# Kernel tuning notes

Hardware: AMD Instinct MI355X
Metric: run time of the kernel (lower is better)

## Reference

```python
import jax, jax.numpy as jnp
import numpy as np

K = 3          # kernel_size
DIL = 2        # dilation
PAD = 2        # unfold padding
EPS = 1e-5     # InstanceNorm eps


def setup_inputs() -> dict:
    key = jax.random.key(0)
    ks = jax.random.split(key, 6)
    b, c, h, w = 8, 128, 128, 128
    c_red = c // 8                      # reduction_ratio = 8
    k2 = K * K
    x = jax.random.normal(ks[0], (b, c, h, w), dtype=jnp.float32)
    # conv1: 1x1, channels -> channels//8, no bias
    w1 = jax.random.normal(ks[1], (c_red, c), dtype=jnp.float32) * (1.0 / np.sqrt(c))
    # InstanceNorm2d affine params
    in_gamma = jnp.ones((c_red,), dtype=jnp.float32)
    in_beta = jnp.zeros((c_red,), dtype=jnp.float32)
    # conv2: 1x1, channels//8 -> k^2 * groups (groups == channels since group_channels=1)
    w2 = jax.random.normal(ks[2], (k2 * c, c_red), dtype=jnp.float32) * (1.0 / np.sqrt(c_red))
    b2 = jnp.zeros((k2 * c,), dtype=jnp.float32)
    return {"x": x, "w1": w1, "in_gamma": in_gamma, "in_beta": in_beta, "w2": w2, "b2": b2}


def reference(x, w1, in_gamma, in_beta, w2, b2):
    b, c, h, w = x.shape
    k2 = K * K
    # --- weight generation branch (stride == 1, ZeroPad2d arg is 0 -> no-op) ---
    t = jnp.einsum('oc,bchw->bohw', w1, x)                      # 1x1 conv, no bias
    mean = t.mean(axis=(2, 3), keepdims=True)                   # InstanceNorm2d (biased var)
    var = t.var(axis=(2, 3), keepdims=True)
    t = (t - mean) * jax.lax.rsqrt(var + EPS)
    t = t * in_gamma[None, :, None, None] + in_beta[None, :, None, None]
    t = jax.nn.relu(t)
    wgt = jnp.einsum('oc,bchw->bohw', w2, t) + b2[None, :, None, None]
    wgt = wgt.reshape(b, c, k2, h, w)                           # (b, groups=c, k^2, h, w)
    # --- unfold: dilated 3x3 patches, padding=2 -> same spatial size ---
    xp = jnp.pad(x, ((0, 0), (0, 0), (PAD, PAD), (PAD, PAD)))
    patches = jnp.stack(
        [xp[:, :, DIL * i:DIL * i + h, DIL * j:DIL * j + w]
         for i in range(K) for j in range(K)], axis=2)          # (b, c, k^2, h, w)
    # --- dynamic-weight multiply + reduce over kernel taps ---
    return (wgt * patches).sum(axis=2)                          # (b, c, h, w)
```

## Files before the change

kernel.cpp:

```cpp
#include <hip/hip_runtime.h>

#define BB   8
#define CC   128
#define CR   16
#define HH   128
#define WW   128
#define HWSZ 16384
#define K2   9
#define NFRAG 72

typedef _Float16 f16x8 __attribute__((ext_vector_type(8)));
typedef float    f32x4 __attribute__((ext_vector_type(4)));

#define WS_PART   0
#define WS_TRAWLO 16384
#define WS_TRAWHI 540672
#define WS_TNLO   1064960
#define WS_TNHI   1589248
#define WS_AFRAG  2113536

__global__ __launch_bounds__(256) void k_conv1(const float* __restrict__ x,
                                               const float* __restrict__ w1,
                                               const float* __restrict__ w2,
                                               const float* __restrict__ b2,
                                               float* __restrict__ ws) {
    const int bid = blockIdx.x;
    const int tid = threadIdx.x;

    if (bid >= 512) {
        const int id = (bid - 512) * 256 + tid;
        if (id >= NFRAG * 64) return;
        const int lane = id & 63;
        const int frag = id >> 6;
        const int ct = frag / 9, k = frag - ct * 9;
        const int row = lane & 15, lg = lane >> 4;
        f16x8 v;
#pragma unroll
        for (int i = 0; i < 8; ++i) {
            const int kk = lg * 8 + i;
            float w = 0.f;
            if (kk < CR)        w = w2[(size_t)((ct * 16 + row) * K2 + k) * CR + kk];
            else if (kk == CR)  w = b2[(ct * 16 + row) * K2 + k];
            v[i] = (_Float16)w;
        }
        f16x8* dst = (f16x8*)(ws + WS_AFRAG);
        dst[frag * 64 + lane] = v;
        return;
    }

    const int tile = bid & 63;
    const int b    = bid >> 6;
    const int pix  = tile * 256 + tid;

    __shared__ float w1s[CR * CC];
    for (int i = tid; i < CR * CC; i += 256) w1s[i] = w1[i];
    __syncthreads();

    const float* xb = x + (size_t)b * CC * HWSZ + pix;
    float acc[CR];
#pragma unroll
    for (int o = 0; o < CR; ++o) acc[o] = 0.f;

    for (int cin = 0; cin < CC; ++cin) {
        float xv = xb[(size_t)cin * HWSZ];
#pragma unroll
        for (int o = 0; o < CR; ++o)
            acc[o] = fmaf(w1s[o * CC + cin], xv, acc[o]);
    }

    {
        f16x8 lo, hi;
#pragma unroll
        for (int i = 0; i < 8; ++i) {
            lo[i] = (_Float16)acc[i];
            hi[i] = (_Float16)acc[i + 8];
        }
        ((f16x8*)(ws + WS_TRAWLO))[(size_t)b * HWSZ + pix] = lo;
        ((f16x8*)(ws + WS_TRAWHI))[(size_t)b * HWSZ + pix] = hi;
    }

    __shared__ float red[4][CR][2];
    const int lane = tid & 63;
    const int wv   = tid >> 6;
#pragma unroll
    for (int o = 0; o < CR; ++o) {
        float s = acc[o];
        float q = s * s;
#pragma unroll
        for (int off = 32; off > 0; off >>= 1) {
            s += __shfl_down(s, off, 64);
            q += __shfl_down(q, off, 64);
        }
        if (lane == 0) { red[wv][o][0] = s; red[wv][o][1] = q; }
    }
    __syncthreads();
    if (tid < CR) {
        const int o = tid;
        float s = red[0][o][0] + red[1][o][0] + red[2][o][0] + red[3][o][0];
        float q = red[0][o][1] + red[1][o][1] + red[2][o][1] + red[3][o][1];
        const int blk = b * 64 + tile;
        float* part = ws + WS_PART;
        part[blk * 32 + o * 2 + 0] = s;
        part[blk * 32 + o * 2 + 1] = q;
    }
}

__global__ __launch_bounds__(256) void k_norm(const float* __restrict__ ws_in,
                                              const float* __restrict__ gamma,
                                              const float* __restrict__ beta,
                                              float* __restrict__ ws_out) {
    const int tid = threadIdx.x;
    const int p   = blockIdx.x * 256 + tid;
    const int b   = p >> 14;

    const float* part = ws_in + WS_PART;

    __shared__ float sts[CR][2];
    {
        const int o  = tid >> 4;
        const int t4 = tid & 15;
        float s = 0.f, q = 0.f;
        if (o < CR) {
#pragma unroll
            for (int j = 0; j < 4; ++j) {
                const int blk = b * 64 + t4 + j * 16;
                s += part[blk * 32 + o * 2 + 0];
                q += part[blk * 32 + o * 2 + 1];
            }
#pragma unroll
            for (int off = 8; off > 0; off >>= 1) {
                s += __shfl_down(s, off, 16);
                q += __shfl_down(q, off, 16);
            }
            if (t4 == 0) {
                const float mean = s * (1.f / (float)HWSZ);
                const float var  = q * (1.f / (float)HWSZ) - mean * mean;
                const float rstd = rsqrtf(var + 1e-5f);
                const float sc   = gamma[o] * rstd;
                sts[o][0] = sc;
                sts[o][1] = beta[o] - mean * sc;
            }
        }
    }
    __syncthreads();

    const f16x8 lo = ((const f16x8*)(ws_in + WS_TRAWLO))[p];
    const f16x8 hi = ((const f16x8*)(ws_in + WS_TRAWHI))[p];
    f16x8 nlo, nhi;
#pragma unroll
    for (int i = 0; i < 8; ++i) {
        float v0 = fmaf((float)lo[i], sts[i][0],     sts[i][1]);
        float v1 = fmaf((float)hi[i], sts[i + 8][0], sts[i + 8][1]);
        nlo[i] = (_Float16)(v0 > 0.f ? v0 : 0.f);
        nhi[i] = (_Float16)(v1 > 0.f ? v1 : 0.f);
    }
    ((f16x8*)(ws_out + WS_TNLO))[p] = nlo;
    ((f16x8*)(ws_out + WS_TNHI))[p] = nhi;
}

__global__ __launch_bounds__(256) void k_main(const float* __restrict__ x,
                                              const float* __restrict__ ws,
                                              float* __restrict__ out) {
    const int bid = blockIdx.x;
    const int w   = (bid & 7) * 512 + (bid >> 3);
    const int y4    = w & 31;
    const int xhalf = (w >> 5) & 1;
    const int ct    = (w >> 6) & 7;
    const int b     = w >> 9;

    const int tid  = threadIdx.x;
    const int wv   = tid >> 6;
    const int lane = tid & 63;
    const int lg   = lane >> 4;
    const int ln   = lane & 15;
    const int y    = y4 * 4 + wv;

    const f16x8* tp = (const f16x8*)(ws + (lg == 1 ? WS_TNHI : WS_TNLO))
                      + ((size_t)b << 14);
    const int tbase = y * WW + xhalf * 64 + ln;

    f16x8 tnf = {}, tnf_nxt = {};
    if (lg < 2)  tnf = tp[tbase];
    if (lg == 2) tnf[0] = (_Float16)1.f;

    const f16x8* afr = (const f16x8*)(ws + WS_AFRAG) + (size_t)ct * K2 * 64 + lane;
    f16x8 af[K2];
#pragma unroll
    for (int k = 0; k < K2; ++k) af[k] = afr[k * 64];

    const int crow = lg * 4;
    const int cb   = ct * 16 + crow;
    const float* xp = x   + ((size_t)b * CC + cb) * HWSZ;
    float*       op = out + ((size_t)b * CC + cb) * HWSZ;
    const bool yint = (y >= 2) && (y < HH - 2);
    const f32x4 zc = {0.f, 0.f, 0.f, 0.f};

#pragma unroll 1
    for (int g = 0; g < 4; ++g) {
        const int colb = xhalf * 64 + g * 16;
        const int col  = colb + ln;
        const int pix  = y * WW + col;

        if (g < 3 && lg < 2)
            tnf_nxt = tp[tbase + (g + 1) * 16];

        f32x4 acc = {0.f, 0.f, 0.f, 0.f};
        const bool xint = (colb >= 2) && (colb + 17 < WW);

        if (yint && xint) {
            const float* q0 = xp + pix;
            const float* q1 = q0 + HWSZ;
            const float* q2 = q0 + 2 * HWSZ;
            const float* q3 = q0 + 3 * HWSZ;
#pragma unroll
            for (int k = 0; k < K2; ++k) {
                const int d = ((k / 3) * 2 - 2) * WW + ((k % 3) * 2 - 2);
                const f32x4 wg = __builtin_amdgcn_mfma_f32_16x16x32_f16(af[k], tnf, zc, 0, 0, 0);
                acc[0] = fmaf(wg[0], q0[d], acc[0]);
                acc[1] = fmaf(wg[1], q1[d], acc[1]);
                acc[2] = fmaf(wg[2], q2[d], acc[2]);
                acc[3] = fmaf(wg[3], q3[d], acc[3]);
            }
        } else {
            int  xoff[3];
            bool xm[3];
#pragma unroll
            for (int j = 0; j < 3; ++j) {
                const int xx = col + (j * 2 - 2);
                xm[j]   = ((unsigned)xx < (unsigned)WW);
                xoff[j] = xx & (WW - 1);
            }
#pragma unroll
            for (int k = 0; k < K2; ++k) {
                const int yy  = y + ((k / 3) * 2 - 2);
                const int off = ((yy & (HH - 1)) << 7) + xoff[k % 3];
                const float m = (xm[k % 3] && ((unsigned)yy < (unsigned)HH)) ? 1.f : 0.f;
                const f32x4 wg = __builtin_amdgcn_mfma_f32_16x16x32_f16(af[k], tnf, zc, 0, 0, 0);
                acc[0] = fmaf(wg[0], xp[off + 0 * HWSZ] * m, acc[0]);
                acc[1] = fmaf(wg[1], xp[off + 1 * HWSZ] * m, acc[1]);
                acc[2] = fmaf(wg[2], xp[off + 2 * HWSZ] * m, acc[2]);
                acc[3] = fmaf(wg[3], xp[off + 3 * HWSZ] * m, acc[3]);
            }
        }

        float* o = op + pix;
        __builtin_nontemporal_store(acc[0], o + 0 * HWSZ);
        __builtin_nontemporal_store(acc[1], o + 1 * HWSZ);
        __builtin_nontemporal_store(acc[2], o + 2 * HWSZ);
        __builtin_nontemporal_store(acc[3], o + 3 * HWSZ);

        tnf = tnf_nxt;
        if (lg == 2) tnf[0] = (_Float16)1.f;
    }
}

extern "C" void kernel_launch(void* const* d_in, const int* in_sizes, int n_in,
                              void* d_out, int out_size, void* d_ws, size_t ws_size,
                              hipStream_t stream) {
    const float* x     = (const float*)d_in[0];
    const float* w1    = (const float*)d_in[1];
    const float* gamma = (const float*)d_in[2];
    const float* beta  = (const float*)d_in[3];
    const float* w2    = (const float*)d_in[4];
    const float* b2    = (const float*)d_in[5];
    float* out = (float*)d_out;

    float* ws = (float*)d_ws;

    k_conv1<<<530, 256, 0, stream>>>(x, w1, w2, b2, ws);

    k_norm<<<512, 256, 0, stream>>>(ws, gamma, beta, ws);

    k_main<<<4096, 256, 0, stream>>>(x, ws, out);
}
```

Before: 70.04 us.

## Fuse conv1 and instance-norm into one cooperative kernel with grid sync

Merges the conv1 and normalization kernels into a single cooperative launch that keeps conv1 results in registers across a grid-wide barrier. This drops the intermediate write and re-read of the raw fp16 activations and removes one kernel launch. The conv1 loop is also restructured to batch 16 channel loads at a time and read transposed w1 from shared memory as vector loads. It adds grid.sync cost, needs all 530 blocks resident at once, and raises register pressure.

```diff
diff --git a/kernel.cpp b/kernel.cpp
--- a/kernel.cpp
+++ b/kernel.cpp
@@ -1,4 +1,7 @@
 #include <hip/hip_runtime.h>
+#include <hip/hip_cooperative_groups.h>
+
+namespace cg = cooperative_groups;
 
 #define BB   8
 #define CC   128
@@ -12,39 +15,41 @@
 typedef _Float16 f16x8 __attribute__((ext_vector_type(8)));
 typedef float    f32x4 __attribute__((ext_vector_type(4)));
 
-#define WS_PART   0
-#define WS_TRAWLO 16384
-#define WS_TRAWHI 540672
-#define WS_TNLO   1064960
-#define WS_TNHI   1589248
-#define WS_AFRAG  2113536
-
-__global__ __launch_bounds__(256) void k_conv1(const float* __restrict__ x,
-                                               const float* __restrict__ w1,
-                                               const float* __restrict__ w2,
-                                               const float* __restrict__ b2,
-                                               float* __restrict__ ws) {
+#define WS_PART  0
+#define WS_TNLO  16384
+#define WS_TNHI  540672
+#define WS_AFRAG 1064960
+
+__global__ __launch_bounds__(256) void k_pre(const float* __restrict__ x,
+                                             const float* __restrict__ w1,
+                                             const float* __restrict__ w2,
+                                             const float* __restrict__ b2,
+                                             const float* __restrict__ gamma,
+                                             const float* __restrict__ beta,
+                                             float* __restrict__ ws) {
     const int bid = blockIdx.x;
     const int tid = threadIdx.x;
+    cg::grid_group grid = cg::this_grid();
 
     if (bid >= 512) {
         const int id = (bid - 512) * 256 + tid;
-        if (id >= NFRAG * 64) return;
-        const int lane = id & 63;
-        const int frag = id >> 6;
-        const int ct = frag / 9, k = frag - ct * 9;
-        const int row = lane & 15, lg = lane >> 4;
-        f16x8 v;
-#pragma unroll
-        for (int i = 0; i < 8; ++i) {
-            const int kk = lg * 8 + i;
-            float w = 0.f;
-            if (kk < CR)        w = w2[(size_t)((ct * 16 + row) * K2 + k) * CR + kk];
-            else if (kk == CR)  w = b2[(ct * 16 + row) * K2 + k];
-            v[i] = (_Float16)w;
-        }
-        f16x8* dst = (f16x8*)(ws + WS_AFRAG);
-        dst[frag * 64 + lane] = v;
+        if (id < NFRAG * 64) {
+            const int lane = id & 63;
+            const int frag = id >> 6;
+            const int ct = frag / 9, k = frag - ct * 9;
+            const int row = lane & 15, lg = lane >> 4;
+            f16x8 v;
+#pragma unroll
+            for (int i = 0; i < 8; ++i) {
+                const int kk = lg * 8 + i;
+                float w = 0.f;
+                if (kk < CR)        w = w2[(size_t)((ct * 16 + row) * K2 + k) * CR + kk];
+                else if (kk == CR)  w = b2[(ct * 16 + row) * K2 + k];
+                v[i] = (_Float16)w;
+            }
+            ((f16x8*)(ws + WS_AFRAG))[frag * 64 + lane] = v;
+        }
+        grid.sync();
         return;
     }
 
@@ -53,7 +58,8 @@
     const int pix  = tile * 256 + tid;
 
     __shared__ float w1s[CR * CC];
-    for (int i = tid; i < CR * CC; i += 256) w1s[i] = w1[i];
+    for (int i = tid; i < CR * CC; i += 256)
+        w1s[i] = w1[(i & 15) * CC + (i >> 4)];
     __syncthreads();
 
     const float* xb = x + (size_t)b * CC * HWSZ + pix;
@@ -61,101 +67,92 @@
 #pragma unroll
     for (int o = 0; o < CR; ++o) acc[o] = 0.f;
 
-    for (int cin = 0; cin < CC; ++cin) {
-        float xv = xb[(size_t)cin * HWSZ];
-#pragma unroll
-        for (int o = 0; o < CR; ++o)
-            acc[o] = fmaf(w1s[o * CC + cin], xv, acc[o]);
-    }
-
+#pragma unroll 1
+    for (int c0 = 0; c0 < CC; c0 += 16) {
+        float xv[16];
+#pragma unroll
+        for (int u = 0; u < 16; ++u)
+            xv[u] = xb[(size_t)(c0 + u) * HWSZ];
+#pragma unroll
+        for (int u = 0; u < 16; ++u) {
+            const f32x4* wv4 = (const f32x4*)&w1s[(c0 + u) * CR];
+            const f32x4 wa = wv4[0], wb = wv4[1], wc = wv4[2], wd = wv4[3];
+#pragma unroll
+            for (int j = 0; j < 4; ++j) {
+                acc[j]      = fmaf(wa[j], xv[u], acc[j]);
+                acc[4 + j]  = fmaf(wb[j], xv[u], acc[4 + j]);
+                acc[8 + j]  = fmaf(wc[j], xv[u], acc[8 + j]);
+                acc[12 + j] = fmaf(wd[j], xv[u], acc[12 + j]);
+            }
+        }
+    }
+
+    __shared__ float red[4][CR][2];
     {
-        f16x8 lo, hi;
-#pragma unroll
-        for (int i = 0; i < 8; ++i) {
-            lo[i] = (_Float16)acc[i];
-            hi[i] = (_Float16)acc[i + 8];
-        }
-        ((f16x8*)(ws + WS_TRAWLO))[(size_t)b * HWSZ + pix] = lo;
-        ((f16x8*)(ws + WS_TRAWHI))[(size_t)b * HWSZ + pix] = hi;
-    }
-
-    __shared__ float red[4][CR][2];
-    const int lane = tid & 63;
-    const int wv   = tid >> 6;
-#pragma unroll
-    for (int o = 0; o < CR; ++o) {
-        float s = acc[o];
-        float q = s * s;
-#pragma unroll
-        for (int off = 32; off > 0; off >>= 1) {
-            s += __shfl_down(s, off, 64);
-            q += __shfl_down(q, off, 64);
-        }
-        if (lane == 0) { red[wv][o][0] = s; red[wv][o][1] = q; }
-    }
-    __syncthreads();
-    if (tid < CR) {
-        const int o = tid;
-        float s = red[0][o][0] + red[1][o][0] + red[2][o][0] + red[3][o][0];
-        float q = red[0][o][1] + red[1][o][1] + red[2][o][1] + red[3][o][1];
-        const int blk = b * 64 + tile;
-        float* part = ws + WS_PART;
-        part[blk * 32 + o * 2 + 0] = s;
-        part[blk * 32 + o * 2 + 1] = q;
-    }
-}
-
-__global__ __launch_bounds__(256) void k_norm(const float* __restrict__ ws_in,
-                                              const float* __restrict__ gamma,
-                                              const float* __restrict__ beta,
-                                              float* __restrict__ ws_out) {
-    const int tid = threadIdx.x;
-    const int p   = blockIdx.x * 256 + tid;
-    const int b   = p >> 14;
-
-    const float* part = ws_in + WS_PART;
+        const int lane = tid & 63;
+        const int wv   = tid >> 6;
+#pragma unroll
+        for (int o = 0; o < CR; ++o) {
+            float s = acc[o];
+            float q = s * s;
+#pragma unroll
+            for (int off = 32; off > 0; off >>= 1) {
+                s += __shfl_down(s, off, 64);
+                q += __shfl_down(q, off, 64);
+            }
+            if (lane == 0) { red[wv][o][0] = s; red[wv][o][1] = q; }
+        }
+        __syncthreads();
+        if (tid < CR) {
+            const int o = tid;
+            float s = red[0][o][0] + red[1][o][0] + red[2][o][0] + red[3][o][0];
+            float q = red[0][o][1] + red[1][o][1] + red[2][o][1] + red[3][o][1];
+            const int blk = b * 64 + tile;
+            ws[WS_PART + blk * 32 + o * 2 + 0] = s;
+            ws[WS_PART + blk * 32 + o * 2 + 1] = q;
+        }
+    }
+
+    grid.sync();
 
     __shared__ float sts[CR][2];
     {
         const int o  = tid >> 4;
         const int t4 = tid & 15;
         float s = 0.f, q = 0.f;
-        if (o < CR) {
-#pragma unroll
-            for (int j = 0; j < 4; ++j) {
-                const int blk = b * 64 + t4 + j * 16;
-                s += part[blk * 32 + o * 2 + 0];
-                q += part[blk * 32 + o * 2 + 1];
-            }
-#pragma unroll
-            for (int off = 8; off > 0; off >>= 1) {
-                s += __shfl_down(s, off, 16);
-                q += __shfl_down(q, off, 16);
-            }
-            if (t4 == 0) {
-                const float mean = s * (1.f / (float)HWSZ);
-                const float var  = q * (1.f / (float)HWSZ) - mean * mean;
-                const float rstd = rsqrtf(var + 1e-5f);
-                const float sc   = gamma[o] * rstd;
-                sts[o][0] = sc;
-                sts[o][1] = beta[o] - mean * sc;
-            }
+#pragma unroll
+        for (int j = 0; j < 4; ++j) {
+            const int blk = b * 64 + t4 + j * 16;
+            s += ws[WS_PART + blk * 32 + o * 2 + 0];
+            q += ws[WS_PART + blk * 32 + o * 2 + 1];
+        }
+#pragma unroll
+        for (int off = 8; off > 0; off >>= 1) {
+            s += __shfl_down(s, off, 16);
+            q += __shfl_down(q, off, 16);
+        }
+        if (t4 == 0) {
+            const float mean = s * (1.f / (float)HWSZ);
+            const float var  = q * (1.f / (float)HWSZ) - mean * mean;
+            const float rstd = rsqrtf(var + 1e-5f);
+            const float sc   = gamma[o] * rstd;
+            sts[o][0] = sc;
+            sts[o][1] = beta[o] - mean * sc;
         }
     }
     __syncthreads();
 
-    const f16x8 lo = ((const f16x8*)(ws_in + WS_TRAWLO))[p];
-    const f16x8 hi = ((const f16x8*)(ws_in + WS_TRAWHI))[p];
+    const int p = b * HWSZ + pix;
     f16x8 nlo, nhi;
 #pragma unroll
     for (int i = 0; i < 8; ++i) {
-        float v0 = fmaf((float)lo[i], sts[i][0],     sts[i][1]);
-        float v1 = fmaf((float)hi[i], sts[i + 8][0], sts[i + 8][1]);
+        float v0 = fmaf(acc[i],     sts[i][0],     sts[i][1]);
+        float v1 = fmaf(acc[i + 8], sts[i + 8][0], sts[i + 8][1]);
         nlo[i] = (_Float16)(v0 > 0.f ? v0 : 0.f);
         nhi[i] = (_Float16)(v1 > 0.f ? v1 : 0.f);
     }
-    ((f16x8*)(ws_out + WS_TNLO))[p] = nlo;
-    ((f16x8*)(ws_out + WS_TNHI))[p] = nhi;
+    ((f16x8*)(ws + WS_TNLO))[p] = nlo;
+    ((f16x8*)(ws + WS_TNHI))[p] = nhi;
 }
 
 __global__ __launch_bounds__(256) void k_main(const float* __restrict__ x,
@@ -264,12 +261,12 @@
     const float* w2    = (const float*)d_in[4];
     const float* b2    = (const float*)d_in[5];
     float* out = (float*)d_out;
-
-    float* ws = (float*)d_ws;
-
-    k_conv1<<<530, 256, 0, stream>>>(x, w1, w2, b2, ws);
-
-    k_norm<<<512, 256, 0, stream>>>(ws, gamma, beta, ws);
+    float* ws  = (float*)d_ws;
+
+    void* args[7] = {(void*)&x, (void*)&w1, (void*)&w2, (void*)&b2,
+                     (void*)&gamma, (void*)&beta, (void*)&ws};
+    hipLaunchCooperativeKernel((const void*)k_pre, dim3(530), dim3(256),
+                               args, 0, stream);
 
     k_main<<<4096, 256, 0, stream>>>(x, ws, out);
 }
```

Result: slower. 117.3 us, median of 4 (+67.5%).
